# Kernel optimization log

Measured on AMD Instinct MI355X. Metric: run time of the kernel, lower is better.

Reference implementation:

```python
import jax, jax.numpy as jnp
import numpy as np

B, D, N = 16, 512, 1024


def setup_inputs() -> dict:
    key = jax.random.key(0)
    k1, k2, k3, k4, k5 = jax.random.split(key, 5)
    return {
        "src_embedding": jax.random.normal(k1, (B, D, N), dtype=jnp.float32),
        "tgt_embedding": jax.random.normal(k2, (B, D, N), dtype=jnp.float32),
        "src": jax.random.normal(k3, (B, 3, N), dtype=jnp.float32),
        "tgt": jax.random.normal(k4, (B, 3, N), dtype=jnp.float32),
        "temperature": jax.random.uniform(k5, (B,), dtype=jnp.float32),
    }


def reference(src_embedding, tgt_embedding, src, tgt, temperature):
    b, d, n = src_embedding.shape
    # scores = softmax(temp * (src_emb^T tgt_emb) / sqrt(d_k), dim=2)
    logits = jnp.einsum("bdn,bdm->bnm", src_embedding, tgt_embedding) / np.sqrt(d).astype(np.float32)
    scores = jax.nn.softmax(temperature.reshape(b, 1, 1) * logits, axis=2)  # [B,N,N]
    # src_corr = tgt @ scores^T  -> soft correspondences [B,3,N]
    src_corr = jnp.einsum("bdm,bnm->bdn", tgt, scores)
    src_mean = src.mean(axis=2, keepdims=True)            # [B,3,1]
    corr_mean = src_corr.mean(axis=2, keepdims=True)      # [B,3,1]
    src_c = src - src_mean
    corr_c = src_corr - corr_mean
    H = jnp.einsum("bin,bjn->bij", src_c, corr_c)         # [B,3,3] covariance
    # Kabsch with reflection fix (batched 3x3 SVD)
    u, s, vh = jnp.linalg.svd(H)
    v = jnp.swapaxes(vh, -1, -2)
    ut = jnp.swapaxes(u, -1, -2)
    det = jax.lax.stop_gradient(jnp.linalg.det(v @ ut))   # +/-1, constant in torch (.item())
    d3 = jnp.stack([jnp.ones_like(det), jnp.ones_like(det), det], axis=-1)  # [B,3]
    R = (v * d3[:, None, :]) @ ut                          # v @ diag(1,1,det) @ u^T
    t = (-R @ src_mean) + corr_mean                        # [B,3,1]
    return R, t.reshape(b, 3)
```

## Files before the change

### kernel.cpp

```cpp
#include <hip/hip_runtime.h>
#include <math.h>

#define BATCH 16
#define DIM 512
#define NPTS 1024

typedef __attribute__((ext_vector_type(8))) short short8;
typedef __attribute__((ext_vector_type(4))) float f32x4;

__device__ __forceinline__ unsigned short f2bf(float x) {
    unsigned u = __float_as_uint(x);
    unsigned r = (u + 0x7FFFu + ((u >> 16) & 1u)) >> 16;
    return (unsigned short)r;
}

__device__ __forceinline__ void load_lds16(const void* g, void* l) {
    __builtin_amdgcn_global_load_lds(
        (const __attribute__((address_space(1))) void*)g,
        (__attribute__((address_space(3))) void*)l, 16, 0, 0);
}

__device__ void kabsch_from_H(double H[3][3], const double sm[3], const double cm[3],
                              float* out, int b) {
    double C[3][3];
    for (int i = 0; i < 3; ++i)
        for (int j = 0; j < 3; ++j) {
            double s = 0;
            for (int k = 0; k < 3; ++k) s += H[k][i] * H[k][j];
            C[i][j] = s;
        }
    double V[3][3] = {{1, 0, 0}, {0, 1, 0}, {0, 0, 1}};
    for (int sweep = 0; sweep < 30; ++sweep) {
        const double offd = fabs(C[0][1]) + fabs(C[0][2]) + fabs(C[1][2]);
        const double diag = fabs(C[0][0]) + fabs(C[1][1]) + fabs(C[2][2]);
        if (offd <= 1e-15 * (diag + 1e-300)) break;
        for (int pq = 0; pq < 3; ++pq) {
            const int p = (pq == 2) ? 1 : 0;
            const int q = (pq == 0) ? 1 : 2;
            const double apq = C[p][q];
            if (fabs(apq) < 1e-300) continue;
            const double theta = (C[q][q] - C[p][p]) / (2.0 * apq);
            const double t_ = copysign(1.0, theta) / (fabs(theta) + sqrt(1.0 + theta * theta));
            const double c_ = 1.0 / sqrt(1.0 + t_ * t_);
            const double s_ = t_ * c_;
            const int r = 3 - p - q;
            const double cpp = C[p][p], cqq = C[q][q];
            C[p][p] = cpp - t_ * apq;
            C[q][q] = cqq + t_ * apq;
            C[p][q] = C[q][p] = 0.0;
            const double crp = C[r][p], crq = C[r][q];
            C[r][p] = C[p][r] = c_ * crp - s_ * crq;
            C[r][q] = C[q][r] = s_ * crp + c_ * crq;
            for (int k = 0; k < 3; ++k) {
                const double vkp = V[k][p], vkq = V[k][q];
                V[k][p] = c_ * vkp - s_ * vkq;
                V[k][q] = s_ * vkp + c_ * vkq;
            }
        }
    }
    double lam[3] = {C[0][0], C[1][1], C[2][2]};
    int i0 = 0, i1 = 1, i2 = 2, tswp;
    if (lam[i0] < lam[i1]) { tswp = i0; i0 = i1; i1 = tswp; }
    if (lam[i0] < lam[i2]) { tswp = i0; i0 = i2; i2 = tswp; }
    if (lam[i1] < lam[i2]) { tswp = i1; i1 = i2; i2 = tswp; }

    const double v0[3] = {V[0][i0], V[1][i0], V[2][i0]};
    const double v1[3] = {V[0][i1], V[1][i1], V[2][i1]};
    const double v2[3] = {V[0][i2], V[1][i2], V[2][i2]};
    const double detV = v0[0] * (v1[1] * v2[2] - v1[2] * v2[1])
                      - v0[1] * (v1[0] * v2[2] - v1[2] * v2[0])
                      + v0[2] * (v1[0] * v2[1] - v1[1] * v2[0]);

    double u0[3], u1[3], u2[3];
    for (int i = 0; i < 3; ++i)
        u0[i] = H[i][0] * v0[0] + H[i][1] * v0[1] + H[i][2] * v0[2];
    double n0 = sqrt(u0[0] * u0[0] + u0[1] * u0[1] + u0[2] * u0[2]);
    n0 = fmax(n0, 1e-300);
    u0[0] /= n0; u0[1] /= n0; u0[2] /= n0;
    for (int i = 0; i < 3; ++i)
        u1[i] = H[i][0] * v1[0] + H[i][1] * v1[1] + H[i][2] * v1[2];
    const double d01 = u0[0] * u1[0] + u0[1] * u1[1] + u0[2] * u1[2];
    u1[0] -= d01 * u0[0]; u1[1] -= d01 * u0[1]; u1[2] -= d01 * u0[2];
    double n1 = sqrt(u1[0] * u1[0] + u1[1] * u1[1] + u1[2] * u1[2]);
    n1 = fmax(n1, 1e-300);
    u1[0] /= n1; u1[1] /= n1; u1[2] /= n1;
    u2[0] = u0[1] * u1[2] - u0[2] * u1[1];
    u2[1] = u0[2] * u1[0] - u0[0] * u1[2];
    u2[2] = u0[0] * u1[1] - u0[1] * u1[0];

    double R[3][3];
    for (int a = 0; a < 3; ++a)
        for (int c = 0; c < 3; ++c)
            R[a][c] = v0[a] * u0[c] + v1[a] * u1[c] + detV * v2[a] * u2[c];

    for (int a = 0; a < 3; ++a) {
        const double tv = cm[a] - (R[a][0] * sm[0] + R[a][1] * sm[1] + R[a][2] * sm[2]);
        out[b * 9 + a * 3 + 0] = (float)R[a][0];
        out[b * 9 + a * 3 + 1] = (float)R[a][1];
        out[b * 9 + a * 3 + 2] = (float)R[a][2];
        out[BATCH * 9 + b * 3 + a] = (float)tv;
    }
}

__global__ __launch_bounds__(256) void transpose_bf16_kernel(
    const float* __restrict__ src_emb, const float* __restrict__ tgt_emb,
    unsigned short* __restrict__ AT, unsigned short* __restrict__ BT)
{
    const int bid = blockIdx.x;
    const int b  = bid >> 7;
    const int dt = (bid >> 4) & 7;
    const int nt = bid & 15;
    const int tid = threadIdx.x;

    __shared__ float tile[64][65];

    for (int pass = 0; pass < 2; ++pass) {
        const float* src = pass ? tgt_emb : src_emb;
        unsigned short* dst = pass ? BT : AT;

        const int lr = tid >> 4;
        const int c4 = (tid & 15) * 4;
#pragma unroll
        for (int q = 0; q < 4; ++q) {
            const int dl = lr + q * 16;
            const float4 v = *(const float4*)(src + ((size_t)(b * DIM + dt * 64 + dl)) * NPTS + nt * 64 + c4);
            tile[dl][c4 + 0] = v.x;
            tile[dl][c4 + 1] = v.y;
            tile[dl][c4 + 2] = v.z;
            tile[dl][c4 + 3] = v.w;
        }
        __syncthreads();

#pragma unroll
        for (int s = 0; s < 2; ++s) {
            const int nl = s * 32 + (tid >> 3);
            const int d8 = (tid & 7) * 8;
            union { unsigned short us[8]; uint4 q4; } pk;
#pragma unroll
            for (int k = 0; k < 8; ++k) pk.us[k] = f2bf(tile[d8 + k][nl]);
            *(uint4*)(dst + ((size_t)(b * NPTS + nt * 64 + nl)) * DIM + dt * 64 + d8) = pk.q4;
        }
        __syncthreads();
    }
}

#define AB_BYTES 4096
#define BB_BYTES 16384

__global__ __launch_bounds__(256, 2) void attn_corr_kernel(
    const unsigned short* __restrict__ AT, const unsigned short* __restrict__ BT,
    const float* __restrict__ tgt, const float* __restrict__ temperature,
    float* __restrict__ P)
{
    __shared__ char lds[4 * (AB_BYTES + BB_BYTES)];

    const int bid = blockIdx.x;
    const int b  = bid >> 6;
    const int inner = bid & 63;
    const int qt = inner >> 2;
    const int ms = inner & 3;
    const int tid = threadIdx.x;
    const int lane = tid & 63;
    const int wv = tid >> 6;

    const unsigned short* Abase = AT + ((size_t)b * NPTS + qt * 64) * DIM;
    const unsigned short* Bbase = BT + ((size_t)b * NPTS + ms * 256) * DIM;

    const int a_r  = wv * 16 + (lane >> 2);
    const int a_cl = (lane & 3) ^ ((a_r >> 1) & 3);
    const size_t a_src_off = (size_t)a_r * DIM + a_cl * 8;

    int b_r[4], b_cl[4];
#pragma unroll
    for (int q = 0; q < 4; ++q) {
        b_r[q]  = q * 64 + wv * 16 + (lane >> 2);
        b_cl[q] = (lane & 3) ^ ((b_r[q] >> 1) & 3);
    }

    const int fp = lane & 15;
    const int fg = lane >> 4;

    f32x4 acc[4][4];
#pragma unroll
    for (int kt = 0; kt < 4; ++kt)
#pragma unroll
        for (int qj = 0; qj < 4; ++qj) acc[kt][qj] = (f32x4){0.f, 0.f, 0.f, 0.f};

    char* AbP[4] = {lds, lds + AB_BYTES, lds + 2 * AB_BYTES, lds + 3 * AB_BYTES};
    char* BbP[4] = {lds + 4 * AB_BYTES,
                    lds + 4 * AB_BYTES + BB_BYTES,
                    lds + 4 * AB_BYTES + 2 * BB_BYTES,
                    lds + 4 * AB_BYTES + 3 * BB_BYTES};

#define STAGE(CH, ABUF, BBUF)                                                        \
    {                                                                                \
        const int d0_ = (CH) * 32;                                                   \
        load_lds16(Abase + a_src_off + d0_, (ABUF) + wv * 1024);                     \
        _Pragma("unroll")                                                            \
        for (int q = 0; q < 4; ++q)                                                  \
            load_lds16(Bbase + (size_t)b_r[q] * DIM + d0_ + b_cl[q] * 8,             \
                       (BBUF) + q * 4096 + wv * 1024);                               \
    }

#define COMPUTE(ABUF, BBUF)                                                          \
    {                                                                                \
        short8 kf[4], qf[4];                                                         \
        _Pragma("unroll")                                                            \
        for (int kt = 0; kt < 4; ++kt) {                                             \
            const int r = wv * 64 + kt * 16 + fp;                                    \
            const int cl = fg ^ ((r >> 1) & 3);                                      \
            kf[kt] = *(const short8*)((BBUF) + r * 64 + cl * 16);                    \
        }                                                                            \
        _Pragma("unroll")                                                            \
        for (int qj = 0; qj < 4; ++qj) {                                             \
            const int r = qj * 16 + fp;                                              \
            const int cl = fg ^ ((r >> 1) & 3);                                      \
            qf[qj] = *(const short8*)((ABUF) + r * 64 + cl * 16);                    \
        }                                                                            \
        __builtin_amdgcn_s_setprio(1);                                               \
        _Pragma("unroll")                                                            \
        for (int kt = 0; kt < 4; ++kt)                                               \
            _Pragma("unroll")                                                        \
            for (int qj = 0; qj < 4; ++qj)                                           \
                acc[kt][qj] = __builtin_amdgcn_mfma_f32_16x16x32_bf16(               \
                    kf[kt], qf[qj], acc[kt][qj], 0, 0, 0);                           \
        __builtin_amdgcn_s_setprio(0);                                               \
    }

    STAGE(0, AbP[0], BbP[0]);
    STAGE(1, AbP[1], BbP[1]);
    STAGE(2, AbP[2], BbP[2]);

#pragma unroll
    for (int ch = 0; ch < 16; ++ch) {
        if (ch <= 13)      { asm volatile("s_waitcnt vmcnt(10)" ::: "memory"); }
        else if (ch == 14) { asm volatile("s_waitcnt vmcnt(5)"  ::: "memory"); }
        else               { asm volatile("s_waitcnt vmcnt(0)"  ::: "memory"); }
        __builtin_amdgcn_s_barrier();
        __builtin_amdgcn_sched_barrier(0);
        if (ch + 3 < 16) STAGE(ch + 3, AbP[(ch + 3) & 3], BbP[(ch + 3) & 3]);
        COMPUTE(AbP[ch & 3], BbP[ch & 3]);
        __builtin_amdgcn_sched_barrier(0);
    }

    const float s2 = temperature[b] * (0.04419417382415922f * 1.4426950408889634f);
    const float* tb = tgt + (size_t)b * 3 * NPTS;

    float l[4]  = {0.f, 0.f, 0.f, 0.f};
    float a0[4] = {0.f, 0.f, 0.f, 0.f};
    float a1[4] = {0.f, 0.f, 0.f, 0.f};
    float a2[4] = {0.f, 0.f, 0.f, 0.f};

#pragma unroll
    for (int kt = 0; kt < 4; ++kt) {
        float t0[4], t1[4], t2[4];
#pragma unroll
        for (int reg = 0; reg < 4; ++reg) {
            const int m = ms * 256 + wv * 64 + kt * 16 + fg * 4 + reg;
            t0[reg] = tb[m];
            t1[reg] = tb[NPTS + m];
            t2[reg] = tb[2 * NPTS + m];
        }
#pragma unroll
        for (int qj = 0; qj < 4; ++qj) {
#pragma unroll
            for (int reg = 0; reg < 4; ++reg) {
                const float w = exp2f(acc[kt][qj][reg] * s2);
                l[qj]  += w;
                a0[qj] = fmaf(w, t0[reg], a0[qj]);
                a1[qj] = fmaf(w, t1[reg], a1[qj]);
                a2[qj] = fmaf(w, t2[reg], a2[qj]);
            }
        }
    }

    float* Pb = P + ((size_t)b * 16 + (ms * 4 + wv)) * 4 * NPTS;
#pragma unroll
    for (int qj = 0; qj < 4; ++qj) {
        float lv = l[qj], v0 = a0[qj], v1 = a1[qj], v2 = a2[qj];
        lv += __shfl_xor(lv, 16); lv += __shfl_xor(lv, 32);
        v0 += __shfl_xor(v0, 16); v0 += __shfl_xor(v0, 32);
        v1 += __shfl_xor(v1, 16); v1 += __shfl_xor(v1, 32);
        v2 += __shfl_xor(v2, 16); v2 += __shfl_xor(v2, 32);
        if (fg == 0) {
            const int n = qt * 64 + qj * 16 + fp;
            Pb[0 * NPTS + n] = lv;
            Pb[1 * NPTS + n] = v0;
            Pb[2 * NPTS + n] = v1;
            Pb[3 * NPTS + n] = v2;
        }
    }
}

__global__ __launch_bounds__(256) void merge_reduce_svd_kernel(
    const float* __restrict__ P, const float* __restrict__ src,
    float* __restrict__ out)
{
    const int b = blockIdx.x;
    const int tid = threadIdx.x;

    __shared__ float wred[4][9];
    __shared__ float meansh[6];

    float corr[4][3], sv[4][3];
    float cs0 = 0, cs1 = 0, cs2 = 0, ss0 = 0, ss1 = 0, ss2 = 0;

#pragma unroll
    for (int j = 0; j < 4; ++j) {
        const int n = tid + j * 256;
        float l = 0, a0 = 0, a1 = 0, a2 = 0;
        for (int pp = 0; pp < 16; ++pp) {
            const float* Pb = P + ((size_t)b * 16 + pp) * 4 * NPTS;
            l  += Pb[n];
            a0 += Pb[NPTS + n];
            a1 += Pb[2 * NPTS + n];
            a2 += Pb[3 * NPTS + n];
        }
        const float inv = 1.0f / l;
        corr[j][0] = a0 * inv; corr[j][1] = a1 * inv; corr[j][2] = a2 * inv;
        cs0 += corr[j][0]; cs1 += corr[j][1]; cs2 += corr[j][2];
        sv[j][0] = src[((size_t)b * 3 + 0) * NPTS + n];
        sv[j][1] = src[((size_t)b * 3 + 1) * NPTS + n];
        sv[j][2] = src[((size_t)b * 3 + 2) * NPTS + n];
        ss0 += sv[j][0]; ss1 += sv[j][1]; ss2 += sv[j][2];
    }

#pragma unroll
    for (int off = 1; off < 64; off <<= 1) {
        ss0 += __shfl_xor(ss0, off); ss1 += __shfl_xor(ss1, off); ss2 += __shfl_xor(ss2, off);
        cs0 += __shfl_xor(cs0, off); cs1 += __shfl_xor(cs1, off); cs2 += __shfl_xor(cs2, off);
    }
    const int wave = tid >> 6;
    if ((tid & 63) == 0) {
        wred[wave][0] = ss0; wred[wave][1] = ss1; wred[wave][2] = ss2;
        wred[wave][3] = cs0; wred[wave][4] = cs1; wred[wave][5] = cs2;
    }
    __syncthreads();
    if (tid < 6)
        meansh[tid] = (wred[0][tid] + wred[1][tid] + wred[2][tid] + wred[3][tid]) * (1.0f / NPTS);
    __syncthreads();
    const float sm0 = meansh[0], sm1 = meansh[1], sm2 = meansh[2];
    const float cm0 = meansh[3], cm1 = meansh[4], cm2 = meansh[5];

    float h[9] = {0, 0, 0, 0, 0, 0, 0, 0, 0};
#pragma unroll
    for (int j = 0; j < 4; ++j) {
        const float a0 = sv[j][0] - sm0, a1 = sv[j][1] - sm1, a2 = sv[j][2] - sm2;
        const float b0 = corr[j][0] - cm0, b1 = corr[j][1] - cm1, b2 = corr[j][2] - cm2;
        h[0] += a0 * b0; h[1] += a0 * b1; h[2] += a0 * b2;
        h[3] += a1 * b0; h[4] += a1 * b1; h[5] += a1 * b2;
        h[6] += a2 * b0; h[7] += a2 * b1; h[8] += a2 * b2;
    }
#pragma unroll
    for (int off = 1; off < 64; off <<= 1) {
#pragma unroll
        for (int j = 0; j < 9; ++j) h[j] += __shfl_xor(h[j], off);
    }
    __syncthreads();
    if ((tid & 63) == 0) {
#pragma unroll
        for (int j = 0; j < 9; ++j) wred[wave][j] = h[j];
    }
    __syncthreads();

    if (tid == 0) {
        double H[3][3];
        for (int i = 0; i < 3; ++i)
            for (int j = 0; j < 3; ++j)
                H[i][j] = (double)wred[0][i * 3 + j] + wred[1][i * 3 + j]
                        + wred[2][i * 3 + j] + wred[3][i * 3 + j];
        const double sm[3] = {sm0, sm1, sm2};
        const double cm[3] = {cm0, cm1, cm2};
        kabsch_from_H(H, sm, cm, out, b);
    }
}

__global__ __launch_bounds__(256) void flash_corr_kernel(
    const float* __restrict__ src_emb,
    const float* __restrict__ tgt_emb,
    const float* __restrict__ tgt,
    const float* __restrict__ temperature,
    float* __restrict__ corr)
{
    const int bid = blockIdx.x;
    const int b   = bid & 15;
    const int qt  = bid >> 4;
    const int n0  = qt * 64;
    const int tid = threadIdx.x;
    const int tx  = tid & 15;
    const int ty  = tid >> 4;

    const float scale = temperature[b] * (1.0f / sqrtf((float)DIM));

    __shared__ float As[2][32][64];
    __shared__ float Bs[2][32][64];
    __shared__ float Ts[3][64];

    const float* Abase  = src_emb + (size_t)b * DIM * NPTS + n0;
    const float* Bbatch = tgt_emb + (size_t)b * DIM * NPTS;
    const float* Tbatch = tgt     + (size_t)b * 3 * NPTS;

    const int dr0 = tid >> 4;
    const int dr1 = dr0 + 16;
    const int c4  = (tid & 15) * 4;

    float mrun[4], lpart[4], acc0[4], acc1[4], acc2[4];
#pragma unroll
    for (int r = 0; r < 4; ++r) {
        mrun[r] = -1e30f; lpart[r] = 0.0f;
        acc0[r] = 0.0f; acc1[r] = 0.0f; acc2[r] = 0.0f;
    }

    for (int mt = 0; mt < 16; ++mt) {
        const int m0 = mt * 64;
        const float* Bbase = Bbatch + m0;
        __syncthreads();
        if (tid < 192) {
            const int i = tid >> 6, mc = tid & 63;
            Ts[i][mc] = Tbatch[i * NPTS + m0 + mc];
        }
        {
            float4 a0 = *(const float4*)(Abase + (size_t)dr0 * NPTS + c4);
            float4 a1 = *(const float4*)(Abase + (size_t)dr1 * NPTS + c4);
            float4 b0 = *(const float4*)(Bbase + (size_t)dr0 * NPTS + c4);
            float4 b1 = *(const float4*)(Bbase + (size_t)dr1 * NPTS + c4);
            *(float4*)&As[0][dr0][c4] = a0;
            *(float4*)&As[0][dr1][c4] = a1;
            *(float4*)&Bs[0][dr0][c4] = b0;
            *(float4*)&Bs[0][dr1][c4] = b1;
        }
        __syncthreads();

        float S[4][4];
#pragma unroll
        for (int r = 0; r < 4; ++r)
#pragma unroll
            for (int c = 0; c < 4; ++c) S[r][c] = 0.0f;

        for (int ch = 0; ch < 16; ++ch) {
            const int buf = ch & 1;
            float4 a0n, a1n, b0n, b1n;
            if (ch < 15) {
                const float* Ab = Abase + (size_t)(ch + 1) * 32 * NPTS;
                const float* Bb = Bbase + (size_t)(ch + 1) * 32 * NPTS;
                a0n = *(const float4*)(Ab + (size_t)dr0 * NPTS + c4);
                a1n = *(const float4*)(Ab + (size_t)dr1 * NPTS + c4);
                b0n = *(const float4*)(Bb + (size_t)dr0 * NPTS + c4);
                b1n = *(const float4*)(Bb + (size_t)dr1 * NPTS + c4);
            }
#pragma unroll
            for (int dk = 0; dk < 32; ++dk) {
                const float4 av = *(const float4*)(&As[buf][dk][ty * 4]);
                const float4 bv = *(const float4*)(&Bs[buf][dk][tx * 4]);
                S[0][0] = fmaf(av.x, bv.x, S[0][0]);
                S[0][1] = fmaf(av.x, bv.y, S[0][1]);
                S[0][2] = fmaf(av.x, bv.z, S[0][2]);
                S[0][3] = fmaf(av.x, bv.w, S[0][3]);
                S[1][0] = fmaf(av.y, bv.x, S[1][0]);
                S[1][1] = fmaf(av.y, bv.y, S[1][1]);
                S[1][2] = fmaf(av.y, bv.z, S[1][2]);
                S[1][3] = fmaf(av.y, bv.w, S[1][3]);
                S[2][0] = fmaf(av.z, bv.x, S[2][0]);
                S[2][1] = fmaf(av.z, bv.y, S[2][1]);
                S[2][2] = fmaf(av.z, bv.z, S[2][2]);
                S[2][3] = fmaf(av.z, bv.w, S[2][3]);
                S[3][0] = fmaf(av.w, bv.x, S[3][0]);
                S[3][1] = fmaf(av.w, bv.y, S[3][1]);
                S[3][2] = fmaf(av.w, bv.z, S[3][2]);
                S[3][3] = fmaf(av.w, bv.w, S[3][3]);
            }
            __syncthreads();
            if (ch < 15) {
                *(float4*)&As[buf ^ 1][dr0][c4] = a0n;
                *(float4*)&As[buf ^ 1][dr1][c4] = a1n;
                *(float4*)&Bs[buf ^ 1][dr0][c4] = b0n;
                *(float4*)&Bs[buf ^ 1][dr1][c4] = b1n;
                __syncthreads();
            }
        }

#pragma unroll
        for (int r = 0; r < 4; ++r) {
            float z0 = S[r][0] * scale, z1 = S[r][1] * scale;
            float z2 = S[r][2] * scale, z3 = S[r][3] * scale;
            float mt_ = fmaxf(fmaxf(z0, z1), fmaxf(z2, z3));
#pragma unroll
            for (int off = 1; off < 16; off <<= 1)
                mt_ = fmaxf(mt_, __shfl_xor(mt_, off));
            const float mnew = fmaxf(mrun[r], mt_);
            const float f = expf(mrun[r] - mnew);
            lpart[r] *= f; acc0[r] *= f; acc1[r] *= f; acc2[r] *= f;
            const float w0 = expf(z0 - mnew);
            const float w1 = expf(z1 - mnew);
            const float w2 = expf(z2 - mnew);
            const float w3 = expf(z3 - mnew);
            lpart[r] += w0 + w1 + w2 + w3;
            const int mc = tx * 4;
            acc0[r] += w0 * Ts[0][mc] + w1 * Ts[0][mc+1] + w2 * Ts[0][mc+2] + w3 * Ts[0][mc+3];
            acc1[r] += w0 * Ts[1][mc] + w1 * Ts[1][mc+1] + w2 * Ts[1][mc+2] + w3 * Ts[1][mc+3];
            acc2[r] += w0 * Ts[2][mc] + w1 * Ts[2][mc+1] + w2 * Ts[2][mc+2] + w3 * Ts[2][mc+3];
            mrun[r] = mnew;
        }
    }

#pragma unroll
    for (int r = 0; r < 4; ++r) {
        float l = lpart[r], a0 = acc0[r], a1 = acc1[r], a2 = acc2[r];
#pragma unroll
        for (int off = 1; off < 16; off <<= 1) {
            l  += __shfl_xor(l,  off);
            a0 += __shfl_xor(a0, off);
            a1 += __shfl_xor(a1, off);
            a2 += __shfl_xor(a2, off);
        }
        if (tx == 0) {
            const int n = n0 + ty * 4 + r;
            const float inv = 1.0f / l;
            corr[((size_t)b * 3 + 0) * NPTS + n] = a0 * inv;
            corr[((size_t)b * 3 + 1) * NPTS + n] = a1 * inv;
            corr[((size_t)b * 3 + 2) * NPTS + n] = a2 * inv;
        }
    }
}

__global__ __launch_bounds__(256) void reduce_svd_kernel(
    const float* __restrict__ src,
    const float* __restrict__ corr,
    float* __restrict__ out)
{
    const int b = blockIdx.x;
    const int tid = threadIdx.x;

    __shared__ float wred[4][9];
    __shared__ float meansh[6];

    const float* sp = src  + (size_t)b * 3 * NPTS;
    const float* cp = corr + (size_t)b * 3 * NPTS;

    float ss0 = 0, ss1 = 0, ss2 = 0, cs0 = 0, cs1 = 0, cs2 = 0;
    for (int n = tid; n < NPTS; n += 256) {
        ss0 += sp[n]; ss1 += sp[NPTS + n]; ss2 += sp[2 * NPTS + n];
        cs0 += cp[n]; cs1 += cp[NPTS + n]; cs2 += cp[2 * NPTS + n];
    }
#pragma unroll
    for (int off = 1; off < 64; off <<= 1) {
        ss0 += __shfl_xor(ss0, off); ss1 += __shfl_xor(ss1, off); ss2 += __shfl_xor(ss2, off);
        cs0 += __shfl_xor(cs0, off); cs1 += __shfl_xor(cs1, off); cs2 += __shfl_xor(cs2, off);
    }
    const int wave = tid >> 6;
    if ((tid & 63) == 0) {
        wred[wave][0] = ss0; wred[wave][1] = ss1; wred[wave][2] = ss2;
        wred[wave][3] = cs0; wred[wave][4] = cs1; wred[wave][5] = cs2;
    }
    __syncthreads();
    if (tid < 6)
        meansh[tid] = (wred[0][tid] + wred[1][tid] + wred[2][tid] + wred[3][tid]) * (1.0f / NPTS);
    __syncthreads();
    const float sm0 = meansh[0], sm1 = meansh[1], sm2 = meansh[2];
    const float cm0 = meansh[3], cm1 = meansh[4], cm2 = meansh[5];

    float h[9] = {0, 0, 0, 0, 0, 0, 0, 0, 0};
    for (int n = tid; n < NPTS; n += 256) {
        const float a0 = sp[n] - sm0, a1 = sp[NPTS + n] - sm1, a2 = sp[2 * NPTS + n] - sm2;
        const float b0 = cp[n] - cm0, b1 = cp[NPTS + n] - cm1, b2 = cp[2 * NPTS + n] - cm2;
        h[0] += a0 * b0; h[1] += a0 * b1; h[2] += a0 * b2;
        h[3] += a1 * b0; h[4] += a1 * b1; h[5] += a1 * b2;
        h[6] += a2 * b0; h[7] += a2 * b1; h[8] += a2 * b2;
    }
#pragma unroll
    for (int off = 1; off < 64; off <<= 1) {
#pragma unroll
        for (int j = 0; j < 9; ++j) h[j] += __shfl_xor(h[j], off);
    }
    __syncthreads();
    if ((tid & 63) == 0) {
#pragma unroll
        for (int j = 0; j < 9; ++j) wred[wave][j] = h[j];
    }
    __syncthreads();

    if (tid == 0) {
        double H[3][3];
        for (int i = 0; i < 3; ++i)
            for (int j = 0; j < 3; ++j)
                H[i][j] = (double)wred[0][i * 3 + j] + wred[1][i * 3 + j]
                        + wred[2][i * 3 + j] + wred[3][i * 3 + j];
        const double sm[3] = {sm0, sm1, sm2};
        const double cm[3] = {cm0, cm1, cm2};
        kabsch_from_H(H, sm, cm, out, b);
    }
}

extern "C" void kernel_launch(void* const* d_in, const int* in_sizes, int n_in,
                              void* d_out, int out_size, void* d_ws, size_t ws_size,
                              hipStream_t stream) {
    const float* src_emb = (const float*)d_in[0];
    const float* tgt_emb = (const float*)d_in[1];
    const float* src     = (const float*)d_in[2];
    const float* tgt     = (const float*)d_in[3];
    const float* temp    = (const float*)d_in[4];
    float* out = (float*)d_out;

    const size_t AT_BYTES = (size_t)BATCH * NPTS * DIM * 2;
    const size_t P_BYTES  = (size_t)BATCH * 16 * 4 * NPTS * 4;

    if (ws_size >= 2 * AT_BYTES + P_BYTES) {
        unsigned short* AT = (unsigned short*)d_ws;
        unsigned short* BT = (unsigned short*)((char*)d_ws + AT_BYTES);
        float* P = (float*)((char*)d_ws + 2 * AT_BYTES);

        transpose_bf16_kernel<<<dim3(BATCH * 8 * 16), dim3(256), 0, stream>>>(
            src_emb, tgt_emb, AT, BT);
        attn_corr_kernel<<<dim3(BATCH * 16 * 4), dim3(256), 0, stream>>>(
            AT, BT, tgt, temp, P);
        merge_reduce_svd_kernel<<<dim3(BATCH), dim3(256), 0, stream>>>(P, src, out);
    } else {
        float* corr = (float*)d_ws;
        flash_corr_kernel<<<dim3(BATCH * (NPTS / 64)), dim3(256), 0, stream>>>(
            src_emb, tgt_emb, tgt, temp, corr);
        reduce_svd_kernel<<<dim3(BATCH), dim3(256), 0, stream>>>(src, corr, out);
    }
}
```

Before: 61.09 us.

## Split transpose passes across blocks, remap attention blocks for L2, prefetch tgt

The transpose kernel now gives each of the two passes (src and tgt embeddings) its own block, doubling the grid and removing the sequential second pass and its barriers. The attention kernel's block-index mapping is permuted so that blocks likely to be co-resident across XCDs share the same (batch, m-slice) B tile, aiming for better L2 reuse. The tgt coordinate loads are hoisted before the GEMM loop so their latency overlaps the MFMA work, at the cost of 48 extra live registers per thread, which could hurt occupancy under launch_bounds(256,2).

```diff
diff --git a/kernel.cpp b/kernel.cpp
--- a/kernel.cpp
+++ b/kernel.cpp
@@ -107,40 +107,39 @@
     unsigned short* __restrict__ AT, unsigned short* __restrict__ BT)
 {
     const int bid = blockIdx.x;
-    const int b  = bid >> 7;
-    const int dt = (bid >> 4) & 7;
-    const int nt = bid & 15;
+    const int pass = bid & 1;
+    const int r2 = bid >> 1;
+    const int b  = r2 >> 7;
+    const int dt = (r2 >> 4) & 7;
+    const int nt = r2 & 15;
     const int tid = threadIdx.x;
 
     __shared__ float tile[64][65];
 
-    for (int pass = 0; pass < 2; ++pass) {
-        const float* src = pass ? tgt_emb : src_emb;
-        unsigned short* dst = pass ? BT : AT;
-
-        const int lr = tid >> 4;
-        const int c4 = (tid & 15) * 4;
-#pragma unroll
-        for (int q = 0; q < 4; ++q) {
-            const int dl = lr + q * 16;
-            const float4 v = *(const float4*)(src + ((size_t)(b * DIM + dt * 64 + dl)) * NPTS + nt * 64 + c4);
-            tile[dl][c4 + 0] = v.x;
-            tile[dl][c4 + 1] = v.y;
-            tile[dl][c4 + 2] = v.z;
-            tile[dl][c4 + 3] = v.w;
-        }
-        __syncthreads();
-
-#pragma unroll
-        for (int s = 0; s < 2; ++s) {
-            const int nl = s * 32 + (tid >> 3);
-            const int d8 = (tid & 7) * 8;
-            union { unsigned short us[8]; uint4 q4; } pk;
-#pragma unroll
-            for (int k = 0; k < 8; ++k) pk.us[k] = f2bf(tile[d8 + k][nl]);
-            *(uint4*)(dst + ((size_t)(b * NPTS + nt * 64 + nl)) * DIM + dt * 64 + d8) = pk.q4;
-        }
-        __syncthreads();
+    const float* src = pass ? tgt_emb : src_emb;
+    unsigned short* dst = pass ? BT : AT;
+
+    const int lr = tid >> 4;
+    const int c4 = (tid & 15) * 4;
+#pragma unroll
+    for (int q = 0; q < 4; ++q) {
+        const int dl = lr + q * 16;
+        const float4 v = *(const float4*)(src + ((size_t)(b * DIM + dt * 64 + dl)) * NPTS + nt * 64 + c4);
+        tile[dl][c4 + 0] = v.x;
+        tile[dl][c4 + 1] = v.y;
+        tile[dl][c4 + 2] = v.z;
+        tile[dl][c4 + 3] = v.w;
+    }
+    __syncthreads();
+
+#pragma unroll
+    for (int s = 0; s < 2; ++s) {
+        const int nl = s * 32 + (tid >> 3);
+        const int d8 = (tid & 7) * 8;
+        union { unsigned short us[8]; uint4 q4; } pk;
+#pragma unroll
+        for (int k = 0; k < 8; ++k) pk.us[k] = f2bf(tile[d8 + k][nl]);
+        *(uint4*)(dst + ((size_t)(b * NPTS + nt * 64 + nl)) * DIM + dt * 64 + d8) = pk.q4;
     }
 }
 
@@ -155,10 +154,14 @@
     __shared__ char lds[4 * (AB_BYTES + BB_BYTES)];
 
     const int bid = blockIdx.x;
-    const int b  = bid >> 6;
-    const int inner = bid & 63;
-    const int qt = inner >> 2;
-    const int ms = inner & 3;
+    const int slice = bid & 7;
+    const int j     = bid >> 3;
+    const int pair  = j >> 4;
+    const int qt    = j & 15;
+    const int pidx  = slice * 8 + pair;
+    const int b     = pidx >> 2;
+    const int ms    = pidx & 3;
+
     const int tid = threadIdx.x;
     const int lane = tid & 63;
     const int wv = tid >> 6;
@@ -179,6 +182,20 @@
 
     const int fp = lane & 15;
     const int fg = lane >> 4;
+
+    const float s2 = temperature[b] * (0.04419417382415922f * 1.4426950408889634f);
+    const float* tb = tgt + (size_t)b * 3 * NPTS;
+    float tv0[4][4], tv1[4][4], tv2[4][4];
+#pragma unroll
+    for (int kt = 0; kt < 4; ++kt)
+#pragma unroll
+        for (int reg = 0; reg < 4; ++reg) {
+            const int m = ms * 256 + wv * 64 + kt * 16 + fg * 4 + reg;
+            tv0[kt][reg] = tb[m];
+            tv1[kt][reg] = tb[NPTS + m];
+            tv2[kt][reg] = tb[2 * NPTS + m];
+        }
+    __builtin_amdgcn_sched_barrier(0);
 
     f32x4 acc[4][4];
 #pragma unroll
@@ -243,9 +260,6 @@
         __builtin_amdgcn_sched_barrier(0);
     }
 
-    const float s2 = temperature[b] * (0.04419417382415922f * 1.4426950408889634f);
-    const float* tb = tgt + (size_t)b * 3 * NPTS;
-
     float l[4]  = {0.f, 0.f, 0.f, 0.f};
     float a0[4] = {0.f, 0.f, 0.f, 0.f};
     float a1[4] = {0.f, 0.f, 0.f, 0.f};
@@ -253,23 +267,15 @@
 
 #pragma unroll
     for (int kt = 0; kt < 4; ++kt) {
-        float t0[4], t1[4], t2[4];
-#pragma unroll
-        for (int reg = 0; reg < 4; ++reg) {
-            const int m = ms * 256 + wv * 64 + kt * 16 + fg * 4 + reg;
-            t0[reg] = tb[m];
-            t1[reg] = tb[NPTS + m];
-            t2[reg] = tb[2 * NPTS + m];
-        }
 #pragma unroll
         for (int qj = 0; qj < 4; ++qj) {
 #pragma unroll
             for (int reg = 0; reg < 4; ++reg) {
                 const float w = exp2f(acc[kt][qj][reg] * s2);
                 l[qj]  += w;
-                a0[qj] = fmaf(w, t0[reg], a0[qj]);
-                a1[qj] = fmaf(w, t1[reg], a1[qj]);
-                a2[qj] = fmaf(w, t2[reg], a2[qj]);
+                a0[qj] = fmaf(w, tv0[kt][reg], a0[qj]);
+                a1[qj] = fmaf(w, tv1[kt][reg], a1[qj]);
+                a2[qj] = fmaf(w, tv2[kt][reg], a2[qj]);
             }
         }
     }
@@ -609,7 +615,7 @@
         unsigned short* BT = (unsigned short*)((char*)d_ws + AT_BYTES);
         float* P = (float*)((char*)d_ws + 2 * AT_BYTES);
 
-        transpose_bf16_kernel<<<dim3(BATCH * 8 * 16), dim3(256), 0, stream>>>(
+        transpose_bf16_kernel<<<dim3(2 * BATCH * 8 * 16), dim3(256), 0, stream>>>(
             src_emb, tgt_emb, AT, BT);
         attn_corr_kernel<<<dim3(BATCH * 16 * 4), dim3(256), 0, stream>>>(
             AT, BT, tgt, temp, P);
```

Measured after the change: 58.72 us. -3.9%, faster.
